# Kernel optimization log

Hardware: AMD Instinct MI355X
Metric: run time of the kernel (lower is better)

Reference implementation:

```python
import jax, jax.numpy as jnp
import numpy as np

S, B, I = 512, 32, 512
H, O = 512, 512
TOP_K = 5
TRUNC = 100
EPS = 1e-7
NEG = -1e9


def setup_inputs() -> dict:
    key = jax.random.key(0)
    ks = jax.random.split(key, 12)
    std = 1.0 / np.sqrt(H)
    return {
        "input": jax.random.normal(ks[0], (S, B, I), jnp.float32),
        "h0": jax.random.normal(ks[1], (1, B, H), jnp.float32),
        "c0": jax.random.normal(ks[2], (1, B, H), jnp.float32),
        "mem0": jax.random.normal(ks[3], (1, B, H), jnp.float32),
        # LSTMCell params (PyTorch layout: gates ordered i, f, g, o)
        "w_ih": jax.random.uniform(ks[4], (4 * H, I), jnp.float32, -std, std),
        "w_hh": jax.random.uniform(ks[5], (4 * H, H), jnp.float32, -std, std),
        "b_ih": jax.random.uniform(ks[6], (4 * H,), jnp.float32, -std, std),
        "b_hh": jax.random.uniform(ks[7], (4 * H,), jnp.float32, -std, std),
        # attention scorer, init N(0, 0.01)
        "w_t": jax.random.normal(ks[8], (2 * H, 1), jnp.float32) * 0.01,
        "fc_w": jax.random.uniform(ks[9], (O, 2 * H), jnp.float32, -1.0 / np.sqrt(2 * H), 1.0 / np.sqrt(2 * H)),
        "fc_b": jax.random.uniform(ks[10], (O,), jnp.float32, -1.0 / np.sqrt(2 * H), 1.0 / np.sqrt(2 * H)),
    }


def _sab_forward(input, h0, c0, mem0, w_ih, w_hh, b_ih, b_hh, w_t, fc_w, fc_b):
    seq_len, batch, _ = input.shape
    hid = w_hh.shape[1]
    m0 = mem0.shape[0]
    mmax = m0 + seq_len  # remem_every_k == 1: one append per step
    mem_buf = jnp.zeros((mmax, batch, hid), input.dtype).at[:m0].set(mem0)
    pos = jnp.arange(mmax)

    def step(carry, xs):
        h, c, mem = carry
        x, i = xs
        trunc = ((i + 1) % TRUNC) == 0
        h_in = jnp.where(trunc, jax.lax.stop_gradient(h), h)
        c_in = jnp.where(trunc, jax.lax.stop_gradient(c), c)
        # LSTM cell
        gates = x @ w_ih.T + b_ih + h_in @ w_hh.T + b_hh
        gi, gf, gg, go = jnp.split(gates, 4, axis=1)
        c_new = jax.nn.sigmoid(gf) * c_in + jax.nn.sigmoid(gi) * jnp.tanh(gg)
        h_new = jax.nn.sigmoid(go) * jnp.tanh(c_new)
        # attention over current (valid) memory
        cur = m0 + i  # valid memory entries before appending
        valid = (pos < cur)[:, None]  # (mmax, 1)
        feat = jnp.tanh(jnp.concatenate([jnp.broadcast_to(h_new[None], (mmax, batch, hid)), mem], axis=2))
        scores = jnp.einsum("mbf,fo->mb", feat, w_t)  # (mmax, batch)
        s_mask = jnp.where(valid, scores, NEG)
        kth = jax.lax.top_k(s_mask.T, TOP_K)[0][:, -1]  # (batch,)
        min_valid = jnp.min(jnp.where(valid, scores, jnp.inf), axis=0)
        delta = jnp.where(cur <= TOP_K, min_valid, kth) + EPS
        aw = jnp.clip(s_mask - delta[None, :], 0.0)  # invalid rows -> 0
        aw = aw / (jnp.sum(aw, axis=0, keepdims=True) + EPS)
        m_t = jnp.einsum("mb,mbh->bh", aw, mem)
        h_out = h_new + m_t
        mem = jax.lax.dynamic_update_slice(mem, h_out[None], (cur, 0, 0))
        return (h_out, c_new, mem), (h_out, m_t)

    (h_f, c_f, mem_f), (h_seq, m_seq) = jax.lax.scan(
        step, (h0[0], c0[0], mem_buf), (input, jnp.arange(seq_len)))
    out = jnp.concatenate([h_seq, m_seq], axis=2) @ fc_w.T + fc_b  # (S,B,O)
    return out, h_f[None], c_f[None], mem_f


def reference(input, h0, c0, mem0, w_ih, w_hh, b_ih, b_hh, w_t, fc_w, fc_b):
    return _sab_forward(input, h0, c0, mem0, w_ih, w_hh, b_ih, b_hh, w_t, fc_w, fc_b)
```

## Files before the change

kernel.cpp:

```cpp
#include <hip/hip_runtime.h>

#define SEQ   512
#define NB    32
#define NH    512
#define BH    16384
#define EPSF  1e-7f
#define NWG   64

#define HF_OFF  8388608
#define CF_OFF  8404992
#define MEM_OFF 8421376

#define X0_OFF   0ul
#define X1_OFF   16777216ul
#define WI0_OFF  33554432ul
#define WI1_OFF  35651584ul
#define HH_OFF   37748736ul
#define HMF_OFF  54558720ul
#define MSEQ_OFF 71368704ul
#define FCW_OFF  88145920ul
#define S2P_OFF  89194496ul
#define BAR_OFF  93396992ul
#define GX_OFF   93405184ul

typedef __attribute__((ext_vector_type(8))) short bf16x8;
typedef __attribute__((ext_vector_type(4))) float f32x4;
typedef __attribute__((ext_vector_type(4))) int   i32x4;

__device__ __forceinline__ unsigned short f2bf(float f){
  unsigned u = __float_as_uint(f);
  unsigned r = (u + 0x7fffu + ((u >> 16) & 1u)) >> 16;
  return (unsigned short)r;
}
__device__ __forceinline__ float bf2f(unsigned short h){
  return __uint_as_float(((unsigned)h) << 16);
}
__device__ __forceinline__ float sigmf(float x){ return 1.f/(1.f + __expf(-x)); }
__device__ __forceinline__ float tanhff(float x){
  x = fminf(20.f, fmaxf(-20.f, x));
  float e = __expf(-2.f*x);
  return (1.f - e)/(1.f + e);
}

__device__ __forceinline__ void store16_cc(void* p, i32x4 v){
  asm volatile("global_store_dwordx4 %0, %1, off sc0 sc1" :: "v"(p), "v"(v) : "memory");
}

__global__ void phase0(const float* __restrict__ x, const float* __restrict__ h0,
                       const float* __restrict__ mem0, const float* __restrict__ fcw,
                       const float* __restrict__ wih,
                       unsigned short* __restrict__ x0, unsigned short* __restrict__ x1,
                       unsigned short* __restrict__ wi0, unsigned short* __restrict__ wi1,
                       unsigned short* __restrict__ hh, unsigned short* __restrict__ hmf,
                       unsigned short* __restrict__ fcwb,
                       float* __restrict__ mem_row0, unsigned* __restrict__ bar){
  long i = (long)blockIdx.x * blockDim.x + threadIdx.x;
  if (i < (long)SEQ*BH){
    float v = x[i];
    unsigned short a = f2bf(v);
    x0[i]=a; x1[i]=f2bf(v - bf2f(a));
  }
  if (i < 2048*512){
    float v = wih[i];
    unsigned short a = f2bf(v);
    wi0[i]=a; wi1[i]=f2bf(v - bf2f(a));
  }
  if (i < 512*1024) fcwb[i] = f2bf(fcw[i]);
  if (i < BH){
    float h = h0[i];
    unsigned short a = f2bf(h);
    int b = (int)(i >> 9), col = (int)(i & 511);
    long d = (long)(col>>3)*256 + b*8 + (col&7);
    hh[d]=a; hmf[d]=f2bf(h - bf2f(a));
    mem_row0[i] = mem0[i];
  }
  if (i < 2048) bar[i] = 0u;
}

__launch_bounds__(256)
__global__ void xgemm(const unsigned short* __restrict__ x0, const unsigned short* __restrict__ x1,
                      const unsigned short* __restrict__ wi0, const unsigned short* __restrict__ wi1,
                      const float* __restrict__ bih, const float* __restrict__ bhh,
                      float* __restrict__ gx){
  const int tid = threadIdx.x;
  const int wave = tid >> 6, lane = tid & 63, quad = lane >> 4, ln = lane & 15;
  const int rowb = blockIdx.x*64 + wave*16;
  const int colb = blockIdx.y*64;
  const long aoff = (long)(rowb + ln)*512 + quad*8;
  f32x4 acc[4] = {{0,0,0,0},{0,0,0,0},{0,0,0,0},{0,0,0,0}};
  #pragma unroll 4
  for (int ki = 0; ki < 16; ++ki){
    bf16x8 a0 = *(const bf16x8*)(x0 + aoff + ki*32);
    bf16x8 a1 = *(const bf16x8*)(x1 + aoff + ki*32);
    #pragma unroll
    for (int n = 0; n < 4; ++n){
      long bo = (long)(colb + n*16 + ln)*512 + quad*8 + ki*32;
      bf16x8 b0 = *(const bf16x8*)(wi0 + bo);
      bf16x8 b1 = *(const bf16x8*)(wi1 + bo);
      acc[n] = __builtin_amdgcn_mfma_f32_16x16x32_bf16(a0, b0, acc[n], 0,0,0);
      acc[n] = __builtin_amdgcn_mfma_f32_16x16x32_bf16(a0, b1, acc[n], 0,0,0);
      acc[n] = __builtin_amdgcn_mfma_f32_16x16x32_bf16(a1, b0, acc[n], 0,0,0);
    }
  }
  #pragma unroll
  for (int n = 0; n < 4; ++n){
    int col = colb + n*16 + ln;
    float bias = bih[col] + bhh[col];
    #pragma unroll
    for (int rr = 0; rr < 4; ++rr){
      int row = rowb + quad*4 + rr;
      gx[(long)row*2048 + col] = acc[n][rr] + bias;
    }
  }
}

__launch_bounds__(320, 1)
__global__ void recurrent(unsigned short* __restrict__ hh,
                          unsigned short* __restrict__ hmf,
                          unsigned short* __restrict__ mseq,
                          float* __restrict__ s2p,
                          unsigned* __restrict__ bar,
                          float* __restrict__ dout,
                          const float* __restrict__ gx,
                          const float* __restrict__ whh,
                          const float* __restrict__ wt,
                          const float* __restrict__ c0){
  const int g    = blockIdx.x;
  const int tid  = threadIdx.x;
  const int wave = tid >> 6, lane = tid & 63, quad = lane >> 4, ln = lane & 15;
  const int mtile = wave & 1, ntile = wave >> 1;

  __shared__ float gates_lds[32*33];
  __shared__ float wt_lds[32*5];
  __shared__ int   repl_lds[32];
  __shared__ unsigned hm_lds[256];
  __shared__ float s2_lds[32];

  bf16x8 fW0[16], fW1[16];
  if (wave < 4){
    int cl   = ntile*16 + ln;
    int gate = cl >> 3, jl = cl & 7;
    long grow = (long)(gate*NH + g*8 + jl);
    const float* wh = whh + grow*NH;
    #pragma unroll
    for (int ki = 0; ki < 16; ++ki){
      int k0 = ki*32 + quad*8;
      bf16x8 a, b;
      #pragma unroll
      for (int e = 0; e < 8; ++e){
        float vh = wh[k0+e];
        unsigned short w0 = f2bf(vh);
        a[e] = (short)w0; b[e] = (short)f2bf(vh - bf2f(w0));
      }
      fW0[ki]=a; fW1[ki]=b;
    }
  }

  const int b_  = tid >> 3, jl_ = tid & 7;
  const int jg_ = g*8 + jl_;
  const float wt2 = wt[NH + jg_];
  float* memf = dout + MEM_OFF;
  float creg = 0.f, m0v = 0.f;
  if (tid < 256){
    creg = c0[b_*NH + jg_];
    m0v  = memf[b_*NH + jg_];
  }
  float va0 = 0.f, va1 = 0.f, va2 = 0.f, va3 = 0.f, va4 = 0.f;
  float hoprev = m0v;

  if (tid < 256){
    float v = tanhff(m0v) * wt2;
    v += __shfl_xor(v, 1); v += __shfl_xor(v, 2); v += __shfl_xor(v, 4);
    if (jl_ == 0)
      __hip_atomic_store((unsigned*)(s2p + g*32 + b_), __float_as_uint(v),
                         __ATOMIC_RELAXED, __HIP_MEMORY_SCOPE_AGENT);
  }

  float gxi = 0.f, gxf = 0.f, gxg = 0.f, gxo = 0.f;
  if (tid < 256){
    const float* gxr0 = gx + (long)b_*2048 + jg_;
    gxi = gxr0[0]; gxf = gxr0[512]; gxg = gxr0[1024]; gxo = gxr0[1536];
  }

  float tv0=-3e38f,tv1=-3e38f,tv2=-3e38f,tv3=-3e38f,tv4=-3e38f;

  unsigned epoch = 1u;
  __syncthreads();
  if (tid == 0)
    __hip_atomic_store(&bar[g*32], epoch, __ATOMIC_RELAXED, __HIP_MEMORY_SCOPE_AGENT);
  if (tid < 64){
    while (true){
      unsigned v = __hip_atomic_load(&bar[tid*32], __ATOMIC_RELAXED, __HIP_MEMORY_SCOPE_AGENT);
      if (__all((int)(v >= epoch))) break;
    }
  }
  __syncthreads();

  const int arow = mtile*16 + ln;

  #pragma unroll 1
  for (int t = 0; t < SEQ; ++t){
    if (tid >= 256){
      const int l4 = tid - 256;
      if (l4 < 32){
        const float* sp = s2p + (long)t*2048 + l4;
        float s0=0.f,s1=0.f,s2v=0.f,s3=0.f;
        #pragma unroll
        for (int q = 0; q < 64; q += 4){
          s0  += sp[(q  )*32];
          s1  += sp[(q+1)*32];
          s2v += sp[(q+2)*32];
          s3  += sp[(q+3)*32];
        }
        float s = (s0+s1) + (s2v+s3);
        int repl = -1;
        if (t < 5){
          repl = t;
          if      (t==0) tv0=s;
          else if (t==1) tv1=s;
          else if (t==2) tv2=s;
          else if (t==3) tv3=s;
          else           tv4=s;
        } else {
          float mn = fminf(fminf(fminf(tv0,tv1),fminf(tv2,tv3)),tv4);
          if (s > mn){
            if      (tv0==mn){tv0=s;repl=0;}
            else if (tv1==mn){tv1=s;repl=1;}
            else if (tv2==mn){tv2=s;repl=2;}
            else if (tv3==mn){tv3=s;repl=3;}
            else             {tv4=s;repl=4;}
          }
        }
        int cnt = (t+1 < 5) ? (t+1) : 5;
        float mn = tv0;
        if (cnt>1) mn = fminf(mn, tv1);
        if (cnt>2) mn = fminf(mn, tv2);
        if (cnt>3) mn = fminf(mn, tv3);
        if (cnt>4) mn = fminf(mn, tv4);
        float thr = mn + EPSF;
        float w0 =            fmaxf(tv0-thr,0.f);
        float w1 = (cnt>1) ? fmaxf(tv1-thr,0.f) : 0.f;
        float w2 = (cnt>2) ? fmaxf(tv2-thr,0.f) : 0.f;
        float w3 = (cnt>3) ? fmaxf(tv3-thr,0.f) : 0.f;
        float w4 = (cnt>4) ? fmaxf(tv4-thr,0.f) : 0.f;
        float inv = 1.f/((w0+w1+w2+w3+w4) + EPSF);
        wt_lds[l4*5+0]=w0*inv;
        wt_lds[l4*5+1]=w1*inv;
        wt_lds[l4*5+2]=w2*inv;
        wt_lds[l4*5+3]=w3*inv;
        wt_lds[l4*5+4]=w4*inv;
        repl_lds[l4]=repl;
      }
    } else {
      const unsigned short* p0 = hh  + (long)t*BH + quad*256 + arow*8;
      const unsigned short* p1 = hmf + (long)t*BH + quad*256 + arow*8;
      f32x4 acc0 = {0.f,0.f,0.f,0.f}, acc1 = {0.f,0.f,0.f,0.f};
      #pragma unroll
      for (int ki = 0; ki < 16; ++ki){
        bf16x8 aH = *(const bf16x8*)(p0 + ki*1024);
        bf16x8 aM = *(const bf16x8*)(p1 + ki*1024);
        acc0 = __builtin_amdgcn_mfma_f32_16x16x32_bf16(aH, fW0[ki], acc0, 0,0,0);
        acc1 = __builtin_amdgcn_mfma_f32_16x16x32_bf16(aH, fW1[ki], acc1, 0,0,0);
        if (ki & 1) acc1 = __builtin_amdgcn_mfma_f32_16x16x32_bf16(aM, fW0[ki], acc1, 0,0,0);
        else        acc0 = __builtin_amdgcn_mfma_f32_16x16x32_bf16(aM, fW0[ki], acc0, 0,0,0);
      }
      #pragma unroll
      for (int r = 0; r < 4; ++r){
        int brow = mtile*16 + quad*4 + r;
        gates_lds[brow*33 + ntile*16 + ln] = acc0[r] + acc1[r];
      }
    }
    __syncthreads();

    if (tid < 256){
      float g0 = gates_lds[b_*33 + jl_     ] + gxi;
      float g1 = gates_lds[b_*33 +  8 + jl_] + gxf;
      float g2 = gates_lds[b_*33 + 16 + jl_] + gxg;
      float g3 = gates_lds[b_*33 + 24 + jl_] + gxo;
      float ig = sigmf(g0), fg = sigmf(g1), gg = tanhff(g2), og = sigmf(g3);
      creg = fg*creg + ig*gg;
      float hn = og * tanhff(creg);

      int rp = repl_lds[b_];
      va0 = (rp==0) ? hoprev : va0;
      va1 = (rp==1) ? hoprev : va1;
      va2 = (rp==2) ? hoprev : va2;
      va3 = (rp==3) ? hoprev : va3;
      va4 = (rp==4) ? hoprev : va4;
      float mt = wt_lds[b_*5+0]*va0 + wt_lds[b_*5+1]*va1 + wt_lds[b_*5+2]*va2
               + wt_lds[b_*5+3]*va3 + wt_lds[b_*5+4]*va4;
      float ho = hn + mt;
      long eoff = (long)b_*NH + jg_;
      memf[(long)(t+1)*BH + eoff] = ho;
      unsigned short h0s = f2bf(ho);
      unsigned short h1s = f2bf(ho - bf2f(h0s));
      hm_lds[b_*8 + jl_] = (unsigned)h0s | (((unsigned)h1s) << 16);
      mseq[(long)t*BH + eoff] = f2bf(mt);
      if (t == SEQ-1) dout[HF_OFF + eoff] = ho;
      hoprev = ho;

      {
        float v = tanhff(ho) * wt2;
        v += __shfl_xor(v, 1); v += __shfl_xor(v, 2); v += __shfl_xor(v, 4);
        if (jl_ == 0) s2_lds[b_] = v;
      }

      {
        int tn = (t+1 < SEQ) ? t+1 : t;
        const float* gxr = gx + ((long)tn*32 + b_)*2048 + jg_;
        gxi = gxr[0]; gxf = gxr[512]; gxg = gxr[1024]; gxo = gxr[1536];
      }
    }

    __syncthreads();
    ++epoch;
    if (tid < 64){
      if (tid < 32){
        int b = tid;
        unsigned q0 = hm_lds[b*8+0], q1 = hm_lds[b*8+1], q2 = hm_lds[b*8+2], q3 = hm_lds[b*8+3];
        unsigned q4 = hm_lds[b*8+4], q5 = hm_lds[b*8+5], q6 = hm_lds[b*8+6], q7 = hm_lds[b*8+7];
        i32x4 hi, mi;
        hi[0] = (int)((q0 & 0xffffu) | (q1 << 16));
        hi[1] = (int)((q2 & 0xffffu) | (q3 << 16));
        hi[2] = (int)((q4 & 0xffffu) | (q5 << 16));
        hi[3] = (int)((q6 & 0xffffu) | (q7 << 16));
        mi[0] = (int)((q0 >> 16) | (q1 & 0xffff0000u));
        mi[1] = (int)((q2 >> 16) | (q3 & 0xffff0000u));
        mi[2] = (int)((q4 >> 16) | (q5 & 0xffff0000u));
        mi[3] = (int)((q6 >> 16) | (q7 & 0xffff0000u));
        long d = (long)(t+1)*BH + g*256 + b*8;
        store16_cc(hh  + d, hi);
        store16_cc(hmf + d, mi);
      } else if (tid < 40){
        int q = tid - 32;
        f32x4 svp = *(const f32x4*)&s2_lds[q*4];
        store16_cc(s2p + (long)(t+1)*2048 + g*32 + q*4, __builtin_bit_cast(i32x4, svp));
      }
      asm volatile("s_waitcnt vmcnt(0)" ::: "memory");
      if (tid == 0)
        __hip_atomic_store(&bar[g*32], epoch, __ATOMIC_RELAXED, __HIP_MEMORY_SCOPE_AGENT);
      while (true){
        unsigned v = __hip_atomic_load(&bar[tid*32], __ATOMIC_RELAXED, __HIP_MEMORY_SCOPE_AGENT);
        if (__all((int)(v >= epoch))) break;
      }
    }
    __syncthreads();
  }
  if (tid < 256)
    dout[CF_OFF + (long)b_*NH + jg_] = creg;
}

__launch_bounds__(256)
__global__ void outgemm(const unsigned short* __restrict__ hh,
                        const unsigned short* __restrict__ mseq,
                        const unsigned short* __restrict__ fcwb,
                        const float* __restrict__ fcb,
                        float* __restrict__ out){
  const int tid = threadIdx.x;
  const int wave = tid >> 6, lane = tid & 63, quad = lane >> 4, ln = lane & 15;
  const int wgM = blockIdx.x;
  const int wgN = blockIdx.y;
  const int r = wgM*64 + wave*16 + ln;
  const int s = r >> 5, b = r & 31;
  const unsigned short* pa_h = hh   + (long)(s+1)*BH + quad*256 + b*8;
  const unsigned short* pa_m = mseq + (long)s*BH     + (long)b*NH + quad*8;
  const unsigned short* pb   = fcwb + (long)(wgN*64 + ln)*1024 + quad*8;
  f32x4 accs[4] = {{0,0,0,0},{0,0,0,0},{0,0,0,0},{0,0,0,0}};
  #pragma unroll 4
  for (int ki = 0; ki < 16; ++ki){
    bf16x8 a = *(const bf16x8*)(pa_h + ki*1024);
    #pragma unroll
    for (int n = 0; n < 4; ++n){
      bf16x8 bb = *(const bf16x8*)(pb + (long)n*16*1024 + ki*32);
      accs[n] = __builtin_amdgcn_mfma_f32_16x16x32_bf16(a, bb, accs[n], 0,0,0);
    }
  }
  #pragma unroll 4
  for (int ki = 0; ki < 16; ++ki){
    bf16x8 a = *(const bf16x8*)(pa_m + ki*32);
    #pragma unroll
    for (int n = 0; n < 4; ++n){
      bf16x8 bb = *(const bf16x8*)(pb + 512 + (long)n*16*1024 + ki*32);
      accs[n] = __builtin_amdgcn_mfma_f32_16x16x32_bf16(a, bb, accs[n], 0,0,0);
    }
  }
  #pragma unroll
  for (int n = 0; n < 4; ++n){
    int o = wgN*64 + n*16 + ln;
    float bias = fcb[o];
    #pragma unroll
    for (int rr = 0; rr < 4; ++rr){
      int row = wgM*64 + wave*16 + quad*4 + rr;
      out[(long)row*512 + o] = accs[n][rr] + bias;
    }
  }
}

extern "C" void kernel_launch(void* const* d_in, const int* in_sizes, int n_in,
                              void* d_out, int out_size, void* d_ws, size_t ws_size,
                              hipStream_t stream){
  (void)in_sizes; (void)n_in; (void)out_size; (void)ws_size;
  const float* x    = (const float*)d_in[0];
  const float* h0   = (const float*)d_in[1];
  const float* c0   = (const float*)d_in[2];
  const float* mem0 = (const float*)d_in[3];
  const float* wih  = (const float*)d_in[4];
  const float* whh  = (const float*)d_in[5];
  const float* bih  = (const float*)d_in[6];
  const float* bhh  = (const float*)d_in[7];
  const float* wt   = (const float*)d_in[8];
  const float* fcw  = (const float*)d_in[9];
  const float* fcb  = (const float*)d_in[10];
  float* out = (float*)d_out;
  char* ws = (char*)d_ws;

  unsigned short* x0   = (unsigned short*)(ws + X0_OFF);
  unsigned short* x1   = (unsigned short*)(ws + X1_OFF);
  unsigned short* wi0  = (unsigned short*)(ws + WI0_OFF);
  unsigned short* wi1  = (unsigned short*)(ws + WI1_OFF);
  unsigned short* hh   = (unsigned short*)(ws + HH_OFF);
  unsigned short* hmf  = (unsigned short*)(ws + HMF_OFF);
  unsigned short* mseq = (unsigned short*)(ws + MSEQ_OFF);
  unsigned short* fcwb = (unsigned short*)(ws + FCW_OFF);
  float*          s2p  = (float*)(ws + S2P_OFF);
  unsigned*       bar  = (unsigned*)(ws + BAR_OFF);
  float*          gx   = (float*)(ws + GX_OFF);

  phase0<<<32768, 256, 0, stream>>>(x, h0, mem0, fcw, wih,
                                    x0, x1, wi0, wi1,
                                    hh, hmf, fcwb, out + MEM_OFF, bar);
  xgemm<<<dim3(256, 32), 256, 0, stream>>>(x0, x1, wi0, wi1, bih, bhh, gx);
  recurrent<<<NWG, 320, 0, stream>>>(hh, hmf, mseq, s2p, bar, out,
                                     gx, whh, wt, c0);
  outgemm<<<dim3(256, 8), 256, 0, stream>>>(hh, mseq, fcwb, fcb, out);
}
```

Measured before the change: 3.886 ms.

## Replace per-step global barrier with per-wave flag arrays and double-buffered LDS

Replaces the per-step single-counter grid barrier, and the second __syncthreads after it, with a flag matrix in which every wave of every workgroup publishes its own step counter. Each wave polls the 256 flags it depends on at the top of the next step. The h/hm packing now uses cross-lane shuffles instead of an LDS staging buffer, and each wave stores its own slices of h and s2 directly. Gate, weight and replacement LDS buffers are double-buffered by step parity so the intra-block barrier can be dropped. This targets the serialized barrier latency per recurrent step, at the cost of more polling loads, and it reuses the wi0 workspace region for the flags after xgemm has consumed it.

```diff
diff --git a/kernel.cpp b/kernel.cpp
--- a/kernel.cpp
+++ b/kernel.cpp
@@ -22,10 +22,14 @@
 #define S2P_OFF  89194496ul
 #define BAR_OFF  93396992ul
 #define GX_OFF   93405184ul
+#define BAR2_OFF WI0_OFF
 
 typedef __attribute__((ext_vector_type(8))) short bf16x8;
 typedef __attribute__((ext_vector_type(4))) float f32x4;
 typedef __attribute__((ext_vector_type(4))) int   i32x4;
+
+#define AL(p) __hip_atomic_load((p), __ATOMIC_RELAXED, __HIP_MEMORY_SCOPE_AGENT)
+#define AS(p,v) __hip_atomic_store((p), (v), __ATOMIC_RELAXED, __HIP_MEMORY_SCOPE_AGENT)
 
 __device__ __forceinline__ unsigned short f2bf(float f){
   unsigned u = __float_as_uint(f);
@@ -44,6 +48,9 @@
 
 __device__ __forceinline__ void store16_cc(void* p, i32x4 v){
   asm volatile("global_store_dwordx4 %0, %1, off sc0 sc1" :: "v"(p), "v"(v) : "memory");
+}
+__device__ __forceinline__ void store4_cc(void* p, unsigned v){
+  asm volatile("global_store_dword %0, %1, off sc0 sc1" :: "v"(p), "v"(v) : "memory");
 }
 
 __global__ void phase0(const float* __restrict__ x, const float* __restrict__ h0,
@@ -120,6 +127,7 @@
                           unsigned short* __restrict__ mseq,
                           float* __restrict__ s2p,
                           unsigned* __restrict__ bar,
+                          unsigned* __restrict__ bar2,
                           float* __restrict__ dout,
                           const float* __restrict__ gx,
                           const float* __restrict__ whh,
@@ -130,11 +138,11 @@
   const int wave = tid >> 6, lane = tid & 63, quad = lane >> 4, ln = lane & 15;
   const int mtile = wave & 1, ntile = wave >> 1;
 
-  __shared__ float gates_lds[32*33];
-  __shared__ float wt_lds[32*5];
-  __shared__ int   repl_lds[32];
-  __shared__ unsigned hm_lds[256];
-  __shared__ float s2_lds[32];
+  __shared__ float gates_lds[2][32*33];
+  __shared__ float wt_lds[2][32*5];
+  __shared__ int   repl_lds[2][32];
+
+  if (tid < 256) AS(&bar2[(long)g*256 + tid], 0u);
 
   bf16x8 fW0[16], fW1[16];
   if (wave < 4){
@@ -172,8 +180,7 @@
     float v = tanhff(m0v) * wt2;
     v += __shfl_xor(v, 1); v += __shfl_xor(v, 2); v += __shfl_xor(v, 4);
     if (jl_ == 0)
-      __hip_atomic_store((unsigned*)(s2p + g*32 + b_), __float_as_uint(v),
-                         __ATOMIC_RELAXED, __HIP_MEMORY_SCOPE_AGENT);
+      AS((unsigned*)(s2p + g*32 + b_), __float_as_uint(v));
   }
 
   float gxi = 0.f, gxf = 0.f, gxg = 0.f, gxo = 0.f;
@@ -184,14 +191,12 @@
 
   float tv0=-3e38f,tv1=-3e38f,tv2=-3e38f,tv3=-3e38f,tv4=-3e38f;
 
-  unsigned epoch = 1u;
   __syncthreads();
-  if (tid == 0)
-    __hip_atomic_store(&bar[g*32], epoch, __ATOMIC_RELAXED, __HIP_MEMORY_SCOPE_AGENT);
+  if (tid == 0) AS(&bar[g*32], 1u);
   if (tid < 64){
     while (true){
-      unsigned v = __hip_atomic_load(&bar[tid*32], __ATOMIC_RELAXED, __HIP_MEMORY_SCOPE_AGENT);
-      if (__all((int)(v >= epoch))) break;
+      unsigned v = AL(&bar[tid*32]);
+      if (__all((int)(v >= 1u))) break;
     }
   }
   __syncthreads();
@@ -200,6 +205,17 @@
 
   #pragma unroll 1
   for (int t = 0; t < SEQ; ++t){
+    const int par = t & 1;
+    {
+      const unsigned tt = (unsigned)t;
+      const unsigned* fr = bar2 + (long)g*256 + lane*4;
+      while (true){
+        unsigned f0 = AL(fr+0), f1 = AL(fr+1), f2 = AL(fr+2), f3 = AL(fr+3);
+        bool ok = (f0 >= tt) & (f1 >= tt) & (f2 >= tt) & (f3 >= tt);
+        if (__all((int)ok)) break;
+      }
+    }
+
     if (tid >= 256){
       const int l4 = tid - 256;
       if (l4 < 32){
@@ -244,12 +260,12 @@
         float w3 = (cnt>3) ? fmaxf(tv3-thr,0.f) : 0.f;
         float w4 = (cnt>4) ? fmaxf(tv4-thr,0.f) : 0.f;
         float inv = 1.f/((w0+w1+w2+w3+w4) + EPSF);
-        wt_lds[l4*5+0]=w0*inv;
-        wt_lds[l4*5+1]=w1*inv;
-        wt_lds[l4*5+2]=w2*inv;
-        wt_lds[l4*5+3]=w3*inv;
-        wt_lds[l4*5+4]=w4*inv;
-        repl_lds[l4]=repl;
+        wt_lds[par][l4*5+0]=w0*inv;
+        wt_lds[par][l4*5+1]=w1*inv;
+        wt_lds[par][l4*5+2]=w2*inv;
+        wt_lds[par][l4*5+3]=w3*inv;
+        wt_lds[par][l4*5+4]=w4*inv;
+        repl_lds[par][l4]=repl;
       }
     } else {
       const unsigned short* p0 = hh  + (long)t*BH + quad*256 + arow*8;
@@ -267,58 +283,44 @@
       #pragma unroll
       for (int r = 0; r < 4; ++r){
         int brow = mtile*16 + quad*4 + r;
-        gates_lds[brow*33 + ntile*16 + ln] = acc0[r] + acc1[r];
+        gates_lds[par][brow*33 + ntile*16 + ln] = acc0[r] + acc1[r];
       }
     }
     __syncthreads();
 
     if (tid < 256){
-      float g0 = gates_lds[b_*33 + jl_     ] + gxi;
-      float g1 = gates_lds[b_*33 +  8 + jl_] + gxf;
-      float g2 = gates_lds[b_*33 + 16 + jl_] + gxg;
-      float g3 = gates_lds[b_*33 + 24 + jl_] + gxo;
+      float g0 = gates_lds[par][b_*33 + jl_     ] + gxi;
+      float g1 = gates_lds[par][b_*33 +  8 + jl_] + gxf;
+      float g2 = gates_lds[par][b_*33 + 16 + jl_] + gxg;
+      float g3 = gates_lds[par][b_*33 + 24 + jl_] + gxo;
       float ig = sigmf(g0), fg = sigmf(g1), gg = tanhff(g2), og = sigmf(g3);
       creg = fg*creg + ig*gg;
       float hn = og * tanhff(creg);
 
-      int rp = repl_lds[b_];
+      int rp = repl_lds[par][b_];
       va0 = (rp==0) ? hoprev : va0;
       va1 = (rp==1) ? hoprev : va1;
       va2 = (rp==2) ? hoprev : va2;
       va3 = (rp==3) ? hoprev : va3;
       va4 = (rp==4) ? hoprev : va4;
-      float mt = wt_lds[b_*5+0]*va0 + wt_lds[b_*5+1]*va1 + wt_lds[b_*5+2]*va2
-               + wt_lds[b_*5+3]*va3 + wt_lds[b_*5+4]*va4;
+      float mt = wt_lds[par][b_*5+0]*va0 + wt_lds[par][b_*5+1]*va1
+               + wt_lds[par][b_*5+2]*va2 + wt_lds[par][b_*5+3]*va3
+               + wt_lds[par][b_*5+4]*va4;
       float ho = hn + mt;
-      long eoff = (long)b_*NH + jg_;
-      memf[(long)(t+1)*BH + eoff] = ho;
-      unsigned short h0s = f2bf(ho);
-      unsigned short h1s = f2bf(ho - bf2f(h0s));
-      hm_lds[b_*8 + jl_] = (unsigned)h0s | (((unsigned)h1s) << 16);
-      mseq[(long)t*BH + eoff] = f2bf(mt);
-      if (t == SEQ-1) dout[HF_OFF + eoff] = ho;
-      hoprev = ho;
-
+
+      float sv = tanhff(ho) * wt2;
+      sv += __shfl_xor(sv, 1); sv += __shfl_xor(sv, 2); sv += __shfl_xor(sv, 4);
+
+      unsigned packed = (unsigned)f2bf(ho);
       {
-        float v = tanhff(ho) * wt2;
-        v += __shfl_xor(v, 1); v += __shfl_xor(v, 2); v += __shfl_xor(v, 4);
-        if (jl_ == 0) s2_lds[b_] = v;
-      }
-
-      {
-        int tn = (t+1 < SEQ) ? t+1 : t;
-        const float* gxr = gx + ((long)tn*32 + b_)*2048 + jg_;
-        gxi = gxr[0]; gxf = gxr[512]; gxg = gxr[1024]; gxo = gxr[1536];
-      }
-    }
-
-    __syncthreads();
-    ++epoch;
-    if (tid < 64){
-      if (tid < 32){
-        int b = tid;
-        unsigned q0 = hm_lds[b*8+0], q1 = hm_lds[b*8+1], q2 = hm_lds[b*8+2], q3 = hm_lds[b*8+3];
-        unsigned q4 = hm_lds[b*8+4], q5 = hm_lds[b*8+5], q6 = hm_lds[b*8+6], q7 = hm_lds[b*8+7];
+        unsigned short h1s = f2bf(ho - bf2f((unsigned short)packed));
+        packed |= ((unsigned)h1s) << 16;
+      }
+      unsigned q0 = __shfl(packed, lane*8+0), q1 = __shfl(packed, lane*8+1);
+      unsigned q2 = __shfl(packed, lane*8+2), q3 = __shfl(packed, lane*8+3);
+      unsigned q4 = __shfl(packed, lane*8+4), q5 = __shfl(packed, lane*8+5);
+      unsigned q6 = __shfl(packed, lane*8+6), q7 = __shfl(packed, lane*8+7);
+      if (lane < 8){
         i32x4 hi, mi;
         hi[0] = (int)((q0 & 0xffffu) | (q1 << 16));
         hi[1] = (int)((q2 & 0xffffu) | (q3 << 16));
@@ -328,23 +330,24 @@
         mi[1] = (int)((q2 >> 16) | (q3 & 0xffff0000u));
         mi[2] = (int)((q4 >> 16) | (q5 & 0xffff0000u));
         mi[3] = (int)((q6 >> 16) | (q7 & 0xffff0000u));
-        long d = (long)(t+1)*BH + g*256 + b*8;
+        long d = (long)(t+1)*BH + g*256 + (wave*8 + lane)*8;
         store16_cc(hh  + d, hi);
         store16_cc(hmf + d, mi);
-      } else if (tid < 40){
-        int q = tid - 32;
-        f32x4 svp = *(const f32x4*)&s2_lds[q*4];
-        store16_cc(s2p + (long)(t+1)*2048 + g*32 + q*4, __builtin_bit_cast(i32x4, svp));
-      }
+      }
+      if (jl_ == 0)
+        store4_cc(s2p + (long)(t+1)*2048 + g*32 + b_, __float_as_uint(sv));
       asm volatile("s_waitcnt vmcnt(0)" ::: "memory");
-      if (tid == 0)
-        __hip_atomic_store(&bar[g*32], epoch, __ATOMIC_RELAXED, __HIP_MEMORY_SCOPE_AGENT);
-      while (true){
-        unsigned v = __hip_atomic_load(&bar[tid*32], __ATOMIC_RELAXED, __HIP_MEMORY_SCOPE_AGENT);
-        if (__all((int)(v >= epoch))) break;
-      }
-    }
-    __syncthreads();
+      AS(&bar2[(long)lane*256 + g*4 + wave], (unsigned)(t+1));
+
+      long eoff = (long)b_*NH + jg_;
+      memf[(long)(t+1)*BH + eoff] = ho;
+      mseq[(long)t*BH + eoff] = f2bf(mt);
+      if (t == SEQ-1) dout[HF_OFF + eoff] = ho;
+      hoprev = ho;
+      int tn = (t+1 < SEQ) ? t+1 : t;
+      const float* gxr = gx + ((long)tn*32 + b_)*2048 + jg_;
+      gxi = gxr[0]; gxf = gxr[512]; gxg = gxr[1024]; gxo = gxr[1536];
+    }
   }
   if (tid < 256)
     dout[CF_OFF + (long)b_*NH + jg_] = creg;
@@ -424,13 +427,14 @@
   unsigned short* fcwb = (unsigned short*)(ws + FCW_OFF);
   float*          s2p  = (float*)(ws + S2P_OFF);
   unsigned*       bar  = (unsigned*)(ws + BAR_OFF);
+  unsigned*       bar2 = (unsigned*)(ws + BAR2_OFF);
   float*          gx   = (float*)(ws + GX_OFF);
 
   phase0<<<32768, 256, 0, stream>>>(x, h0, mem0, fcw, wih,
                                     x0, x1, wi0, wi1,
                                     hh, hmf, fcwb, out + MEM_OFF, bar);
   xgemm<<<dim3(256, 32), 256, 0, stream>>>(x0, x1, wi0, wi1, bih, bhh, gx);
-  recurrent<<<NWG, 320, 0, stream>>>(hh, hmf, mseq, s2p, bar, out,
+  recurrent<<<NWG, 320, 0, stream>>>(hh, hmf, mseq, s2p, bar, bar2, out,
                                      gx, whh, wt, c0);
   outgemm<<<dim3(256, 8), 256, 0, stream>>>(hh, mseq, fcwb, fcb, out);
 }
```

Result: slower. 11.16 ms (+187.1%).
